# Optimization experiments

Hardware: AMD Instinct MI355X
Metric: run time of the kernel (lower is better)

Reference implementation:

```python
import jax, jax.numpy as jnp
import numpy as np

N_NODES = 100000
N_EDGES = 1600000
N_GRAPHS = 1000
D_IN = 64
D_HID = 64
D_OUT = 8


def _glorot(k, shape):
    lim = float(np.sqrt(6.0 / (shape[0] + shape[1])))
    return jax.random.uniform(k, shape, jnp.float32, -lim, lim)


def setup_inputs() -> dict:
    key = jax.random.key(0)
    ks = jax.random.split(key, 12)
    x = jax.random.normal(ks[0], (N_NODES, D_IN), jnp.float32)
    edge_index = jax.random.randint(ks[1], (2, N_EDGES), 0, N_NODES, jnp.int32)
    batch = jnp.sort(jax.random.randint(ks[2], (N_NODES,), 0, N_GRAPHS, jnp.int32))
    return {
        "x": x,
        "edge_index": edge_index,
        "batch": batch,
        "W1": _glorot(ks[3], (D_IN, D_HID)),
        "b1": jnp.zeros((D_HID,), jnp.float32),
        "W2": _glorot(ks[4], (D_HID, D_HID)),
        "b2": jnp.zeros((D_HID,), jnp.float32),
        "lw1": _glorot(ks[5], (D_HID, D_HID // 2)),
        "lb1": jnp.zeros((D_HID // 2,), jnp.float32),
        "lw2": _glorot(ks[6], (D_HID // 2, D_OUT)),
        "lb2": jnp.zeros((D_OUT,), jnp.float32),
    }


def reference(x, edge_index, batch, W1, b1, W2, b2, lw1, lb1, lw2, lb2):
    # --- GCN normalization (PyG defaults: add self-loops, sym norm) ---
    loop = jnp.arange(N_NODES, dtype=edge_index.dtype)
    src = jnp.concatenate([edge_index[0], loop])
    dst = jnp.concatenate([edge_index[1], loop])
    deg = jax.ops.segment_sum(jnp.ones_like(dst, jnp.float32), dst, num_segments=N_NODES)
    dinv = jnp.where(deg > 0, jax.lax.rsqrt(jnp.maximum(deg, 1.0)), 0.0)
    norm = dinv[src] * dinv[dst]  # [E+N]

    def gcn_conv(h, W, b):
        h = h @ W  # [N, d]
        msg = h[src] * norm[:, None]  # gather along edges
        return jax.ops.segment_sum(msg, dst, num_segments=N_NODES) + b

    h = jax.nn.relu(gcn_conv(x, W1, b1))
    h = gcn_conv(h, W2, b2)

    # --- global mean pool per graph ---
    counts = jax.ops.segment_sum(jnp.ones((N_NODES,), jnp.float32), batch, num_segments=N_GRAPHS)
    pooled = jax.ops.segment_sum(h, batch, num_segments=N_GRAPHS) / jnp.maximum(counts, 1.0)[:, None]

    # --- MLP head (dropout = identity in eval) ---
    z = jax.nn.relu(pooled @ lw1 + lb1)
    return z @ lw2 + lb2
```

## Files before the change

kernel.cpp:

```cpp
#include <hip/hip_runtime.h>

static constexpr int NN  = 100000;
static constexpr int NE  = 1600000;
static constexpr int NG  = 1000;
static constexpr int D   = 64;
static constexpr int DH  = 32;
static constexpr int DO  = 8;
static constexpr int BKT = 128;
static constexpr int NBK = (NN + BKT - 1) / BKT;
static constexpr int CHUNK = 4096;
static constexpr int NCH = (NE + CHUNK - 1) / CHUNK;

typedef __attribute__((ext_vector_type(8))) short bf16x8;
typedef __attribute__((ext_vector_type(4))) float f32x4;

__device__ __forceinline__ float b2f(unsigned short u) {
    return __uint_as_float(((unsigned int)u) << 16);
}
__device__ __forceinline__ unsigned short f2b(float f) {
    unsigned int u = __float_as_uint(f);
    u += 0x7FFFu + ((u >> 16) & 1u);
    return (unsigned short)(u >> 16);
}
__device__ __forceinline__ uint4 pack8(const unsigned short* h) {
    uint4 u;
    u.x = (unsigned)h[0] | ((unsigned)h[1] << 16);
    u.y = (unsigned)h[2] | ((unsigned)h[3] << 16);
    u.z = (unsigned)h[4] | ((unsigned)h[5] << 16);
    u.w = (unsigned)h[6] | ((unsigned)h[7] << 16);
    return u;
}

__global__ __launch_bounds__(512) void
k_hist(const int* __restrict__ dst, int* __restrict__ cntmat) {
    __shared__ int lcnt[NBK];
    int t = threadIdx.x;
    long base = (long)blockIdx.x * CHUNK;
    for (int b = t; b < NBK; b += 512) lcnt[b] = 0;
    __syncthreads();
#pragma unroll
    for (int j = 0; j < 8; ++j) {
        long i = base + j * 512 + t;
        if (i < NE) atomicAdd(&lcnt[dst[i] >> 7], 1);
    }
    __syncthreads();
    for (int b = t; b < NBK; b += 512)
        cntmat[blockIdx.x * NBK + b] = lcnt[b];
}

__global__ __launch_bounds__(512) void
k_colsum_rowscan(int* __restrict__ cntmat, int* __restrict__ bsum) {
    __shared__ int s[512];
    int b = blockIdx.x, t = threadIdx.x;
    int v = (t < NCH) ? cntmat[t * NBK + b] : 0;
    s[t] = v;
    __syncthreads();
    for (int o = 1; o < 512; o <<= 1) {
        int a = (t >= o) ? s[t - o] : 0;
        __syncthreads();
        s[t] += a;
        __syncthreads();
    }
    if (t < NCH) cntmat[t * NBK + b] = s[t] - v;
    if (t == 0) bsum[b] = s[511];
}

__global__ __launch_bounds__(1024) void
k_scan_prepw(const int* __restrict__ bsum, int* __restrict__ boffs,
             const float* __restrict__ W1, const float* __restrict__ W2,
             unsigned short* __restrict__ wtbuf) {
    int t = threadIdx.x;
    if (blockIdx.x == 0) {
        __shared__ int s[1024];
        int v = (t < NBK) ? bsum[t] : 0;
        s[t] = v;
        __syncthreads();
        for (int o = 1; o < 1024; o <<= 1) {
            int a = (t >= o) ? s[t - o] : 0;
            __syncthreads();
            s[t] += a;
            __syncthreads();
        }
        if (t < NBK) boffs[t] = s[t] - v;
        if (t == 0) boffs[NBK] = NE;
    } else if (t < 256) {
        const float* W = (blockIdx.x == 2) ? W2 : W1;
        unsigned short* WtHi = wtbuf + (size_t)(blockIdx.x - 1) * 8192;
        unsigned short* WtLo = WtHi + 4096;
        int n = t >> 2, k0 = (t & 3) * 16;
        unsigned short hi[16], lo[16];
#pragma unroll
        for (int i = 0; i < 16; ++i) {
            float v = W[(k0 + i) * 64 + n];
            hi[i] = f2b(v);
            lo[i] = f2b(v - b2f(hi[i]));
        }
        ((uint4*)WtHi)[n * 8 + (t & 3) * 2]     = pack8(hi);
        ((uint4*)WtHi)[n * 8 + (t & 3) * 2 + 1] = pack8(hi + 8);
        ((uint4*)WtLo)[n * 8 + (t & 3) * 2]     = pack8(lo);
        ((uint4*)WtLo)[n * 8 + (t & 3) * 2 + 1] = pack8(lo + 8);
    }
}

__global__ __launch_bounds__(512) void
k_bin(const int* __restrict__ src, const int* __restrict__ dst,
      const int* __restrict__ cntmat, const int* __restrict__ boffs,
      int* __restrict__ ebuf) {
    __shared__ int lcnt[NBK];
    __shared__ int lbase[NBK];
    int t = threadIdx.x;
    long base = (long)blockIdx.x * CHUNK;
    for (int b = t; b < NBK; b += 512) lcnt[b] = 0;
    __syncthreads();
    int pk[8], bk[8], of[8];
#pragma unroll
    for (int j = 0; j < 8; ++j) {
        long i = base + j * 512 + t;
        if (i < NE) {
            int d = dst[i];
            bk[j] = d >> 7;
            pk[j] = src[i] * BKT + (d & (BKT - 1));
            of[j] = atomicAdd(&lcnt[bk[j]], 1);
        } else bk[j] = -1;
    }
    __syncthreads();
    for (int b = t; b < NBK; b += 512)
        lbase[b] = cntmat[blockIdx.x * NBK + b] + boffs[b];
    __syncthreads();
#pragma unroll
    for (int j = 0; j < 8; ++j)
        if (bk[j] >= 0) ebuf[lbase[bk[j]] + of[j]] = pk[j];
}

__global__ __launch_bounds__(512) void
k_csrdeg(const int* __restrict__ boffs, const int* __restrict__ ebuf,
         int* __restrict__ rowptr, float* __restrict__ dinv, int* __restrict__ csr) {
    __shared__ int hist[BKT];
    __shared__ int sc[BKT];
    __shared__ int lcur[BKT];
    int b = blockIdx.x, t = threadIdx.x;
    if (t < BKT) hist[t] = 0;
    __syncthreads();
    int beg = boffs[b], end = boffs[b + 1];
    for (int e = beg + t; e < end; e += 512)
        atomicAdd(&hist[ebuf[e] & (BKT - 1)], 1);
    __syncthreads();
    if (t < BKT) sc[t] = hist[t];
    __syncthreads();
    for (int o = 1; o < BKT; o <<= 1) {
        int a = (t < BKT && t >= o) ? sc[t - o] : 0;
        __syncthreads();
        if (t < BKT) sc[t] += a;
        __syncthreads();
    }
    int v0 = b * BKT;
    if (t < BKT) {
        int v = v0 + t;
        if (v < NN) {
            int excl = beg + sc[t] - hist[t];
            rowptr[v] = excl;
            dinv[v]   = rsqrtf((float)(hist[t] + 1));
            lcur[t]   = excl;
        }
    }
    if (b == NBK - 1 && t == 0) rowptr[NN] = NE;
    __syncthreads();
    for (int e = beg + t; e < end; e += 512) {
        int p = ebuf[e];
        int slot = atomicAdd(&lcur[p & (BKT - 1)], 1);
        csr[slot] = p >> 7;
    }
}

template <bool SPLIT_A>
__global__ __launch_bounds__(256) void
k_mm_mfma(const void* __restrict__ Ain, const unsigned short* __restrict__ wt,
          const float* __restrict__ dinv, uint4* __restrict__ out) {
    __shared__ unsigned short smem[4 * 64 * 72];
    unsigned short* Ahi  = smem;
    unsigned short* Alo  = smem + 4608;
    unsigned short* WtHi = smem + 9216;
    unsigned short* WtLo = smem + 13824;
    int t = threadIdx.x;
    int r = t >> 2, cc = t & 3, c0 = cc * 16;
    long n0 = (long)blockIdx.x * 64;
    {
        const uint4* H = (const uint4*)wt;
        const uint4* L = (const uint4*)(wt + 4096);
        uint4* dh = (uint4*)&WtHi[r * 72 + c0];
        uint4* dl = (uint4*)&WtLo[r * 72 + c0];
        dh[0] = H[r * 8 + cc * 2]; dh[1] = H[r * 8 + cc * 2 + 1];
        dl[0] = L[r * 8 + cc * 2]; dl[1] = L[r * 8 + cc * 2 + 1];
    }
    {
        long n = n0 + r; if (n >= NN) n = NN - 1;
        if constexpr (SPLIT_A) {
            const float4* X = (const float4*)Ain;
            unsigned short hi[16], lo[16];
#pragma unroll
            for (int i = 0; i < 4; ++i) {
                float4 v = X[n * 16 + cc * 4 + i];
                float vv[4] = {v.x, v.y, v.z, v.w};
#pragma unroll
                for (int j = 0; j < 4; ++j) {
                    unsigned short h = f2b(vv[j]);
                    hi[i * 4 + j] = h;
                    lo[i * 4 + j] = f2b(vv[j] - b2f(h));
                }
            }
            uint4* dh = (uint4*)&Ahi[r * 72 + c0];
            uint4* dl = (uint4*)&Alo[r * 72 + c0];
            dh[0] = pack8(hi); dh[1] = pack8(hi + 8);
            dl[0] = pack8(lo); dl[1] = pack8(lo + 8);
        } else {
            const uint4* X = (const uint4*)Ain;
            uint4* dh = (uint4*)&Ahi[r * 72 + c0];
            dh[0] = X[n * 8 + cc * 2]; dh[1] = X[n * 8 + cc * 2 + 1];
        }
    }
    __syncthreads();
    int lane = t & 63, w = t >> 6;
    int q = lane >> 4, m = lane & 15;
    f32x4 acc[4] = {{0.f,0.f,0.f,0.f},{0.f,0.f,0.f,0.f},{0.f,0.f,0.f,0.f},{0.f,0.f,0.f,0.f}};
#pragma unroll
    for (int s = 0; s < 2; ++s) {
        int ko = s * 32 + q * 8;
        bf16x8 ah = *(const bf16x8*)&Ahi[(w * 16 + m) * 72 + ko];
        bf16x8 al{};
        if constexpr (SPLIT_A) al = *(const bf16x8*)&Alo[(w * 16 + m) * 72 + ko];
#pragma unroll
        for (int c = 0; c < 4; ++c) {
            bf16x8 bh = *(const bf16x8*)&WtHi[(c * 16 + m) * 72 + ko];
            bf16x8 bl = *(const bf16x8*)&WtLo[(c * 16 + m) * 72 + ko];
            acc[c] = __builtin_amdgcn_mfma_f32_16x16x32_bf16(ah, bh, acc[c], 0, 0, 0);
            acc[c] = __builtin_amdgcn_mfma_f32_16x16x32_bf16(ah, bl, acc[c], 0, 0, 0);
            if constexpr (SPLIT_A)
                acc[c] = __builtin_amdgcn_mfma_f32_16x16x32_bf16(al, bh, acc[c], 0, 0, 0);
        }
    }
    __syncthreads();
    float* Ct = (float*)smem;
#pragma unroll
    for (int c = 0; c < 4; ++c)
#pragma unroll
        for (int rr = 0; rr < 4; ++rr)
            Ct[(w * 16 + q * 4 + rr) * 68 + c * 16 + m] = acc[c][rr];
    __syncthreads();
    {
        long n = n0 + r;
        if (n < NN) {
            float dv = dinv[n];
            unsigned short ob[16];
#pragma unroll
            for (int i = 0; i < 4; ++i) {
                float4 v = *(const float4*)&Ct[r * 68 + c0 + i * 4];
                ob[i * 4 + 0] = f2b(v.x * dv); ob[i * 4 + 1] = f2b(v.y * dv);
                ob[i * 4 + 2] = f2b(v.z * dv); ob[i * 4 + 3] = f2b(v.w * dv);
            }
            out[n * 8 + cc * 2]     = pack8(ob);
            out[n * 8 + cc * 2 + 1] = pack8(ob + 8);
        }
    }
}

template <bool RELU>
__global__ __launch_bounds__(256) void
k_agg(const int* __restrict__ rowptr, const int* __restrict__ csr,
      const uint4* __restrict__ g4, const float* __restrict__ dinv,
      const float* __restrict__ bias, uint4* __restrict__ out4) {
    int t = threadIdx.x;
    int lane = t & 63;
    int fg = lane & 7;
    int slot = lane >> 3;
    int wid = blockIdx.x * 4 + (t >> 6);
    int v = wid * 8 + slot;
    int beg = rowptr[v];
    int len = rowptr[v + 1] - beg;
    int lmax = len;
    lmax = max(lmax, __shfl_xor(lmax, 8));
    lmax = max(lmax, __shfl_xor(lmax, 16));
    lmax = max(lmax, __shfl_xor(lmax, 32));
    float acc[8];
    {
        uint4 sv = g4[(long)v * 8 + fg];
        acc[0] = __uint_as_float(sv.x << 16); acc[1] = __uint_as_float(sv.x & 0xFFFF0000u);
        acc[2] = __uint_as_float(sv.y << 16); acc[3] = __uint_as_float(sv.y & 0xFFFF0000u);
        acc[4] = __uint_as_float(sv.z << 16); acc[5] = __uint_as_float(sv.z & 0xFFFF0000u);
        acc[6] = __uint_as_float(sv.w << 16); acc[7] = __uint_as_float(sv.w & 0xFFFF0000u);
    }
    for (int e = 0; e < lmax; e += 8) {
#pragma unroll
        for (int j = 0; j < 8; ++j) {
            int ee = e + j;
            float m = (ee < len) ? 1.f : 0.f;
            int idx = beg + ((ee < len) ? ee : 0);
            int srcn = csr[idx];
            uint4 a = g4[(long)srcn * 8 + fg];
            acc[0] += m * __uint_as_float(a.x << 16);
            acc[1] += m * __uint_as_float(a.x & 0xFFFF0000u);
            acc[2] += m * __uint_as_float(a.y << 16);
            acc[3] += m * __uint_as_float(a.y & 0xFFFF0000u);
            acc[4] += m * __uint_as_float(a.z << 16);
            acc[5] += m * __uint_as_float(a.z & 0xFFFF0000u);
            acc[6] += m * __uint_as_float(a.w << 16);
            acc[7] += m * __uint_as_float(a.w & 0xFFFF0000u);
        }
    }
    float dv = dinv[v];
    unsigned short ob[8];
#pragma unroll
    for (int k = 0; k < 8; ++k) {
        float x = acc[k] * dv + bias[fg * 8 + k];
        if (RELU) x = fmaxf(x, 0.f);
        ob[k] = f2b(x);
    }
    out4[(long)v * 8 + fg] = pack8(ob);
}

__global__ void k_poolhead(const unsigned short* __restrict__ h,
                           const int* __restrict__ batch,
                           const float* __restrict__ lw1, const float* __restrict__ lb1,
                           const float* __restrict__ lw2, const float* __restrict__ lb2,
                           float* __restrict__ out) {
    __shared__ float pl[D];
    __shared__ float z[DH];
    int g = blockIdx.x;
    int t = threadIdx.x;
    int lo = 0, hi = NN;
    while (lo < hi) { int m = (lo + hi) >> 1; if (batch[m] < g) lo = m + 1; else hi = m; }
    int lb = lo;
    hi = NN;
    while (lo < hi) { int m = (lo + hi) >> 1; if (batch[m] < g + 1) lo = m + 1; else hi = m; }
    int ub = lo;
    float s = 0.f;
    int n = lb;
    for (; n + 4 <= ub; n += 4) {
        float a0 = b2f(h[(long)(n + 0) * D + t]);
        float a1 = b2f(h[(long)(n + 1) * D + t]);
        float a2 = b2f(h[(long)(n + 2) * D + t]);
        float a3 = b2f(h[(long)(n + 3) * D + t]);
        s += a0 + a1 + a2 + a3;
    }
    for (; n < ub; ++n) s += b2f(h[(long)n * D + t]);
    pl[t] = s / fmaxf((float)(ub - lb), 1.0f);
    __syncthreads();
    if (t < DH) {
        float a = lb1[t];
#pragma unroll
        for (int k = 0; k < D; ++k) a += pl[k] * lw1[k * DH + t];
        z[t] = fmaxf(a, 0.f);
    }
    __syncthreads();
    if (t < DO) {
        float a = lb2[t];
#pragma unroll
        for (int j = 0; j < DH; ++j) a += z[j] * lw2[j * DO + t];
        out[g * DO + t] = a;
    }
}

extern "C" void kernel_launch(void* const* d_in, const int* in_sizes, int n_in,
                              void* d_out, int out_size, void* d_ws, size_t ws_size,
                              hipStream_t stream) {
    const float* x    = (const float*)d_in[0];
    const int*   ei   = (const int*)  d_in[1];
    const int*   batch= (const int*)  d_in[2];
    const float* W1   = (const float*)d_in[3];
    const float* b1   = (const float*)d_in[4];
    const float* W2   = (const float*)d_in[5];
    const float* b2   = (const float*)d_in[6];
    const float* lw1  = (const float*)d_in[7];
    const float* lb1  = (const float*)d_in[8];
    const float* lw2  = (const float*)d_in[9];
    const float* lb2  = (const float*)d_in[10];
    float* out = (float*)d_out;

    const int* srcv = ei;
    const int* dstv = ei + NE;

    char* ws = (char*)d_ws;
    size_t off = 0;
    auto alloc = [&](size_t bytes) {
        void* p = ws + off;
        off = (off + bytes + 255) & ~(size_t)255;
        return p;
    };
    int*   cntmat = (int*)  alloc((size_t)NCH * NBK * 4);
    int*   bsum   = (int*)  alloc((size_t)NBK * 4);
    int*   boffs  = (int*)  alloc((size_t)(NBK + 1) * 4);
    int*   rowptr = (int*)  alloc((size_t)(NN + 1) * 4);
    int*   csr    = (int*)  alloc((size_t)NE * 4);
    float* dinv   = (float*)alloc((size_t)NN * 4);
    unsigned short* wtbuf = (unsigned short*)alloc((size_t)4 * 4096 * 2);
    unsigned short* bufA = (unsigned short*)alloc((size_t)NN * D * 2);
    unsigned short* bufB = (unsigned short*)alloc((size_t)NN * D * 2);
    int*   ebuf   = (int*)bufA;

    k_hist          <<<NCH, 512, 0, stream>>>(dstv, cntmat);
    k_colsum_rowscan<<<NBK, 512, 0, stream>>>(cntmat, bsum);
    k_scan_prepw    <<<3, 1024, 0, stream>>>(bsum, boffs, W1, W2, wtbuf);
    k_bin           <<<NCH, 512, 0, stream>>>(srcv, dstv, cntmat, boffs, ebuf);
    k_csrdeg        <<<NBK, 512, 0, stream>>>(boffs, ebuf, rowptr, dinv, csr);

    const int MMB = (NN + 63) / 64;

    k_mm_mfma<true><<<MMB, 256, 0, stream>>>(x, wtbuf, dinv, (uint4*)bufA);
    k_agg<true><<<NN / 32, 256, 0, stream>>>(
        rowptr, csr, (const uint4*)bufA, dinv, b1, (uint4*)bufB);

    k_mm_mfma<false><<<MMB, 256, 0, stream>>>(bufB, wtbuf + 8192, dinv, (uint4*)bufA);
    k_agg<false><<<NN / 32, 256, 0, stream>>>(
        rowptr, csr, (const uint4*)bufA, dinv, b2, (uint4*)bufB);

    k_poolhead<<<NG, 64, 0, stream>>>(bufB, batch, lw1, lb1, lw2, lb2, out);
}
```

Before: 225.4 us.

## Merge CSR build into cooperative kernel and fuse layer-1 aggregation with layer-2 matmul

The five CSR-construction kernels (histogram, column scan, bucket offsets, binning, per-bucket sort and degree) become one cooperative kernel that uses grid-wide syncs, which removes several launch gaps. The first aggregation is fused with the second layer's MFMA matmul, so the ReLU'd hidden features stay in LDS and are never written to and re-read from global memory. This cuts launch overhead and one full feature round trip. In exchange it relies on a cooperative launch of 391 blocks of 512 threads all being resident at once, grid.sync costs, and a 512-thread fused kernel whose occupancy may be lower than before.

```diff
diff --git a/kernel.cpp b/kernel.cpp
--- a/kernel.cpp
+++ b/kernel.cpp
@@ -1,4 +1,7 @@
 #include <hip/hip_runtime.h>
+#include <hip/hip_cooperative_groups.h>
+
+namespace cg = cooperative_groups;
 
 static constexpr int NN  = 100000;
 static constexpr int NE  = 1600000;
@@ -32,60 +35,64 @@
 }
 
 __global__ __launch_bounds__(512) void
-k_hist(const int* __restrict__ dst, int* __restrict__ cntmat) {
-    __shared__ int lcnt[NBK];
-    int t = threadIdx.x;
-    long base = (long)blockIdx.x * CHUNK;
-    for (int b = t; b < NBK; b += 512) lcnt[b] = 0;
-    __syncthreads();
-#pragma unroll
-    for (int j = 0; j < 8; ++j) {
-        long i = base + j * 512 + t;
-        if (i < NE) atomicAdd(&lcnt[dst[i] >> 7], 1);
-    }
-    __syncthreads();
-    for (int b = t; b < NBK; b += 512)
-        cntmat[blockIdx.x * NBK + b] = lcnt[b];
-}
-
-__global__ __launch_bounds__(512) void
-k_colsum_rowscan(int* __restrict__ cntmat, int* __restrict__ bsum) {
-    __shared__ int s[512];
-    int b = blockIdx.x, t = threadIdx.x;
-    int v = (t < NCH) ? cntmat[t * NBK + b] : 0;
-    s[t] = v;
-    __syncthreads();
-    for (int o = 1; o < 512; o <<= 1) {
-        int a = (t >= o) ? s[t - o] : 0;
-        __syncthreads();
-        s[t] += a;
-        __syncthreads();
-    }
-    if (t < NCH) cntmat[t * NBK + b] = s[t] - v;
-    if (t == 0) bsum[b] = s[511];
-}
-
-__global__ __launch_bounds__(1024) void
-k_scan_prepw(const int* __restrict__ bsum, int* __restrict__ boffs,
-             const float* __restrict__ W1, const float* __restrict__ W2,
-             unsigned short* __restrict__ wtbuf) {
-    int t = threadIdx.x;
-    if (blockIdx.x == 0) {
-        __shared__ int s[1024];
-        int v = (t < NBK) ? bsum[t] : 0;
-        s[t] = v;
+k_prep(const int* __restrict__ src, const int* __restrict__ dst,
+       const float* __restrict__ W1, const float* __restrict__ W2,
+       int* __restrict__ cntmat, int* __restrict__ bsum, int* __restrict__ boffs,
+       unsigned short* __restrict__ wtbuf, int* __restrict__ ebuf,
+       int* __restrict__ rowptr, float* __restrict__ dinv, int* __restrict__ csr) {
+    cg::grid_group grid = cg::this_grid();
+    __shared__ int sh[1568];
+    int t = threadIdx.x, blk = blockIdx.x;
+
+    {
+        for (int b = t; b < NBK; b += 512) sh[b] = 0;
+        __syncthreads();
+        long base = (long)blk * CHUNK;
+#pragma unroll
+        for (int j = 0; j < 8; ++j) {
+            long i = base + j * 512 + t;
+            if (i < NE) atomicAdd(&sh[dst[i] >> 7], 1);
+        }
+        __syncthreads();
+        for (int b = t; b < NBK; b += 512) cntmat[blk * NBK + b] = sh[b];
+    }
+    grid.sync();
+
+    for (int bb = 0; bb < 2; ++bb) {
+        int b = blk + bb * 391;
+        int v = (t < NCH) ? cntmat[t * NBK + b] : 0;
+        __syncthreads();
+        sh[t] = v;
+        __syncthreads();
+        for (int o = 1; o < 512; o <<= 1) {
+            int a = (t >= o) ? sh[t - o] : 0;
+            __syncthreads();
+            sh[t] += a;
+            __syncthreads();
+        }
+        if (t < NCH) cntmat[t * NBK + b] = sh[t] - v;
+        if (t == 0) bsum[b] = sh[511];
+    }
+    grid.sync();
+
+    if (blk == 0) {
+        int v0 = (t < NBK) ? bsum[t] : 0;
+        int v1 = (t + 512 < NBK) ? bsum[t + 512] : 0;
+        sh[t] = v0; sh[t + 512] = v1;
         __syncthreads();
         for (int o = 1; o < 1024; o <<= 1) {
-            int a = (t >= o) ? s[t - o] : 0;
+            int a0 = (t >= o) ? sh[t - o] : 0;
+            int a1 = sh[t + 512 - o];
             __syncthreads();
-            s[t] += a;
+            sh[t] += a0; sh[t + 512] += a1;
             __syncthreads();
         }
-        if (t < NBK) boffs[t] = s[t] - v;
+        if (t < NBK) boffs[t] = sh[t] - v0;
+        if (t + 512 < NBK) boffs[t + 512] = sh[t + 512] - v1;
         if (t == 0) boffs[NBK] = NE;
-    } else if (t < 256) {
-        const float* W = (blockIdx.x == 2) ? W2 : W1;
-        unsigned short* WtHi = wtbuf + (size_t)(blockIdx.x - 1) * 8192;
+    } else if (blk <= 2 && t < 256) {
+        const float* W = (blk == 2) ? W2 : W1;
+        unsigned short* WtHi = wtbuf + (size_t)(blk - 1) * 8192;
         unsigned short* WtLo = WtHi + 4096;
         int n = t >> 2, k0 = (t & 3) * 16;
         unsigned short hi[16], lo[16];
@@ -100,81 +107,77 @@
         ((uint4*)WtLo)[n * 8 + (t & 3) * 2]     = pack8(lo);
         ((uint4*)WtLo)[n * 8 + (t & 3) * 2 + 1] = pack8(lo + 8);
     }
-}
-
-__global__ __launch_bounds__(512) void
-k_bin(const int* __restrict__ src, const int* __restrict__ dst,
-      const int* __restrict__ cntmat, const int* __restrict__ boffs,
-      int* __restrict__ ebuf) {
-    __shared__ int lcnt[NBK];
-    __shared__ int lbase[NBK];
-    int t = threadIdx.x;
-    long base = (long)blockIdx.x * CHUNK;
-    for (int b = t; b < NBK; b += 512) lcnt[b] = 0;
-    __syncthreads();
-    int pk[8], bk[8], of[8];
-#pragma unroll
-    for (int j = 0; j < 8; ++j) {
-        long i = base + j * 512 + t;
-        if (i < NE) {
-            int d = dst[i];
-            bk[j] = d >> 7;
-            pk[j] = src[i] * BKT + (d & (BKT - 1));
-            of[j] = atomicAdd(&lcnt[bk[j]], 1);
-        } else bk[j] = -1;
-    }
-    __syncthreads();
-    for (int b = t; b < NBK; b += 512)
-        lbase[b] = cntmat[blockIdx.x * NBK + b] + boffs[b];
-    __syncthreads();
-#pragma unroll
-    for (int j = 0; j < 8; ++j)
-        if (bk[j] >= 0) ebuf[lbase[bk[j]] + of[j]] = pk[j];
-}
-
-__global__ __launch_bounds__(512) void
-k_csrdeg(const int* __restrict__ boffs, const int* __restrict__ ebuf,
-         int* __restrict__ rowptr, float* __restrict__ dinv, int* __restrict__ csr) {
-    __shared__ int hist[BKT];
-    __shared__ int sc[BKT];
-    __shared__ int lcur[BKT];
-    int b = blockIdx.x, t = threadIdx.x;
-    if (t < BKT) hist[t] = 0;
-    __syncthreads();
-    int beg = boffs[b], end = boffs[b + 1];
-    for (int e = beg + t; e < end; e += 512)
-        atomicAdd(&hist[ebuf[e] & (BKT - 1)], 1);
-    __syncthreads();
-    if (t < BKT) sc[t] = hist[t];
-    __syncthreads();
-    for (int o = 1; o < BKT; o <<= 1) {
-        int a = (t < BKT && t >= o) ? sc[t - o] : 0;
-        __syncthreads();
-        if (t < BKT) sc[t] += a;
-        __syncthreads();
-    }
-    int v0 = b * BKT;
-    if (t < BKT) {
-        int v = v0 + t;
-        if (v < NN) {
-            int excl = beg + sc[t] - hist[t];
-            rowptr[v] = excl;
-            dinv[v]   = rsqrtf((float)(hist[t] + 1));
-            lcur[t]   = excl;
-        }
-    }
-    if (b == NBK - 1 && t == 0) rowptr[NN] = NE;
-    __syncthreads();
-    for (int e = beg + t; e < end; e += 512) {
-        int p = ebuf[e];
-        int slot = atomicAdd(&lcur[p & (BKT - 1)], 1);
-        csr[slot] = p >> 7;
-    }
-}
-
-template <bool SPLIT_A>
+    grid.sync();
+
+    {
+        int* lcnt  = sh;
+        int* lbase = sh + 784;
+        for (int b = t; b < NBK; b += 512) lcnt[b] = 0;
+        __syncthreads();
+        long base = (long)blk * CHUNK;
+        int pk[8], bk[8], of[8];
+#pragma unroll
+        for (int j = 0; j < 8; ++j) {
+            long i = base + j * 512 + t;
+            if (i < NE) {
+                int d = dst[i];
+                bk[j] = d >> 7;
+                pk[j] = src[i] * BKT + (d & (BKT - 1));
+                of[j] = atomicAdd(&lcnt[bk[j]], 1);
+            } else bk[j] = -1;
+        }
+        __syncthreads();
+        for (int b = t; b < NBK; b += 512)
+            lbase[b] = cntmat[blk * NBK + b] + boffs[b];
+        __syncthreads();
+#pragma unroll
+        for (int j = 0; j < 8; ++j)
+            if (bk[j] >= 0) ebuf[lbase[bk[j]] + of[j]] = pk[j];
+    }
+    grid.sync();
+
+    for (int bb = 0; bb < 2; ++bb) {
+        int b = blk + bb * 391;
+        int* hist = sh;
+        int* sc   = sh + 128;
+        int* lcur = sh + 256;
+        __syncthreads();
+        if (t < BKT) hist[t] = 0;
+        __syncthreads();
+        int beg = boffs[b], end = boffs[b + 1];
+        for (int e = beg + t; e < end; e += 512)
+            atomicAdd(&hist[ebuf[e] & (BKT - 1)], 1);
+        __syncthreads();
+        if (t < BKT) sc[t] = hist[t];
+        __syncthreads();
+        for (int o = 1; o < BKT; o <<= 1) {
+            int a = (t < BKT && t >= o) ? sc[t - o] : 0;
+            __syncthreads();
+            if (t < BKT) sc[t] += a;
+            __syncthreads();
+        }
+        int v0 = b * BKT;
+        if (t < BKT) {
+            int v = v0 + t;
+            if (v < NN) {
+                int excl = beg + sc[t] - hist[t];
+                rowptr[v] = excl;
+                dinv[v]   = rsqrtf((float)(hist[t] + 1));
+                lcur[t]   = excl;
+            }
+        }
+        if (b == NBK - 1 && t == 0) rowptr[NN] = NE;
+        __syncthreads();
+        for (int e = beg + t; e < end; e += 512) {
+            int p = ebuf[e];
+            int slot = atomicAdd(&lcur[p & (BKT - 1)], 1);
+            csr[slot] = p >> 7;
+        }
+    }
+}
+
 __global__ __launch_bounds__(256) void
-k_mm_mfma(const void* __restrict__ Ain, const unsigned short* __restrict__ wt,
+k_mm_mfma(const float* __restrict__ Ain, const unsigned short* __restrict__ wt,
           const float* __restrict__ dinv, uint4* __restrict__ out) {
     __shared__ unsigned short smem[4 * 64 * 72];
     unsigned short* Ahi  = smem;
@@ -194,29 +197,23 @@
     }
     {
         long n = n0 + r; if (n >= NN) n = NN - 1;
-        if constexpr (SPLIT_A) {
-            const float4* X = (const float4*)Ain;
-            unsigned short hi[16], lo[16];
-#pragma unroll
-            for (int i = 0; i < 4; ++i) {
-                float4 v = X[n * 16 + cc * 4 + i];
-                float vv[4] = {v.x, v.y, v.z, v.w};
-#pragma unroll
-                for (int j = 0; j < 4; ++j) {
-                    unsigned short h = f2b(vv[j]);
-                    hi[i * 4 + j] = h;
-                    lo[i * 4 + j] = f2b(vv[j] - b2f(h));
-                }
+        const float4* X = (const float4*)Ain;
+        unsigned short hi[16], lo[16];
+#pragma unroll
+        for (int i = 0; i < 4; ++i) {
+            float4 v = X[n * 16 + cc * 4 + i];
+            float vv[4] = {v.x, v.y, v.z, v.w};
+#pragma unroll
+            for (int j = 0; j < 4; ++j) {
+                unsigned short h = f2b(vv[j]);
+                hi[i * 4 + j] = h;
+                lo[i * 4 + j] = f2b(vv[j] - b2f(h));
             }
-            uint4* dh = (uint4*)&Ahi[r * 72 + c0];
-            uint4* dl = (uint4*)&Alo[r * 72 + c0];
-            dh[0] = pack8(hi); dh[1] = pack8(hi + 8);
-            dl[0] = pack8(lo); dl[1] = pack8(lo + 8);
-        } else {
-            const uint4* X = (const uint4*)Ain;
-            uint4* dh = (uint4*)&Ahi[r * 72 + c0];
-            dh[0] = X[n * 8 + cc * 2]; dh[1] = X[n * 8 + cc * 2 + 1];
-        }
+        }
+        uint4* dh = (uint4*)&Ahi[r * 72 + c0];
+        uint4* dl = (uint4*)&Alo[r * 72 + c0];
+        dh[0] = pack8(hi); dh[1] = pack8(hi + 8);
+        dl[0] = pack8(lo); dl[1] = pack8(lo + 8);
     }
     __syncthreads();
     int lane = t & 63, w = t >> 6;
@@ -226,16 +223,14 @@
     for (int s = 0; s < 2; ++s) {
         int ko = s * 32 + q * 8;
         bf16x8 ah = *(const bf16x8*)&Ahi[(w * 16 + m) * 72 + ko];
-        bf16x8 al{};
-        if constexpr (SPLIT_A) al = *(const bf16x8*)&Alo[(w * 16 + m) * 72 + ko];
+        bf16x8 al = *(const bf16x8*)&Alo[(w * 16 + m) * 72 + ko];
 #pragma unroll
         for (int c = 0; c < 4; ++c) {
             bf16x8 bh = *(const bf16x8*)&WtHi[(c * 16 + m) * 72 + ko];
             bf16x8 bl = *(const bf16x8*)&WtLo[(c * 16 + m) * 72 + ko];
             acc[c] = __builtin_amdgcn_mfma_f32_16x16x32_bf16(ah, bh, acc[c], 0, 0, 0);
             acc[c] = __builtin_amdgcn_mfma_f32_16x16x32_bf16(ah, bl, acc[c], 0, 0, 0);
-            if constexpr (SPLIT_A)
-                acc[c] = __builtin_amdgcn_mfma_f32_16x16x32_bf16(al, bh, acc[c], 0, 0, 0);
+            acc[c] = __builtin_amdgcn_mfma_f32_16x16x32_bf16(al, bh, acc[c], 0, 0, 0);
         }
     }
     __syncthreads();
@@ -263,26 +258,42 @@
     }
 }
 
-template <bool RELU>
-__global__ __launch_bounds__(256) void
-k_agg(const int* __restrict__ rowptr, const int* __restrict__ csr,
-      const uint4* __restrict__ g4, const float* __restrict__ dinv,
-      const float* __restrict__ bias, uint4* __restrict__ out4) {
+__global__ __launch_bounds__(512) void
+k_aggmm(const int* __restrict__ rowptr, const int* __restrict__ csr,
+        const uint4* __restrict__ g4, const float* __restrict__ dinv,
+        const float* __restrict__ bias, const unsigned short* __restrict__ wt,
+        uint4* __restrict__ out) {
+    __shared__ unsigned short smem[3 * 4608];
+    unsigned short* Ahi  = smem;
+    unsigned short* WtHi = smem + 4608;
+    unsigned short* WtLo = smem + 9216;
     int t = threadIdx.x;
-    int lane = t & 63;
-    int fg = lane & 7;
-    int slot = lane >> 3;
-    int wid = blockIdx.x * 4 + (t >> 6);
-    int v = wid * 8 + slot;
-    int beg = rowptr[v];
-    int len = rowptr[v + 1] - beg;
+    long n0 = (long)blockIdx.x * 64;
+    if (t < 256) {
+        int r = t >> 2, cc = t & 3, c0 = cc * 16;
+        const uint4* H = (const uint4*)wt;
+        const uint4* L = (const uint4*)(wt + 4096);
+        uint4* dh = (uint4*)&WtHi[r * 72 + c0];
+        uint4* dl = (uint4*)&WtLo[r * 72 + c0];
+        dh[0] = H[r * 8 + cc * 2]; dh[1] = H[r * 8 + cc * 2 + 1];
+        dl[0] = L[r * 8 + cc * 2]; dl[1] = L[r * 8 + cc * 2 + 1];
+    }
+    int lane = t & 63, w = t >> 6;
+    int fg = lane & 7, slot = lane >> 3;
+    int ln = w * 8 + slot;
+    long v = n0 + ln;
+    int vc = (v < NN) ? (int)v : NN - 1;
+    int beg = rowptr[vc];
+    int len = rowptr[vc + 1] - beg;
+    if (v >= NN) len = 0;
     int lmax = len;
     lmax = max(lmax, __shfl_xor(lmax, 8));
     lmax = max(lmax, __shfl_xor(lmax, 16));
     lmax = max(lmax, __shfl_xor(lmax, 32));
     float acc[8];
     {
-        uint4 sv = g4[(long)v * 8 + fg];
+        uint4 sv = g4[(long)vc * 8 + fg];
+        if (v >= NN) { sv.x = sv.y = sv.z = sv.w = 0u; }
         acc[0] = __uint_as_float(sv.x << 16); acc[1] = __uint_as_float(sv.x & 0xFFFF0000u);
         acc[2] = __uint_as_float(sv.y << 16); acc[3] = __uint_as_float(sv.y & 0xFFFF0000u);
         acc[4] = __uint_as_float(sv.z << 16); acc[5] = __uint_as_float(sv.z & 0xFFFF0000u);
@@ -306,14 +317,102 @@
             acc[7] += m * __uint_as_float(a.w & 0xFFFF0000u);
         }
     }
+    {
+        float dv = dinv[vc];
+        unsigned short ob[8];
+#pragma unroll
+        for (int k = 0; k < 8; ++k) {
+            float x = fmaxf(acc[k] * dv + bias[fg * 8 + k], 0.f);
+            ob[k] = f2b(x);
+        }
+        *(uint4*)&Ahi[ln * 72 + fg * 8] = pack8(ob);
+    }
+    __syncthreads();
+    int q = lane >> 4, m = lane & 15;
+    int rs = (w & 3) * 16;
+    int cb0 = (w >> 2) * 2;
+    f32x4 c2[2] = {{0.f,0.f,0.f,0.f},{0.f,0.f,0.f,0.f}};
+#pragma unroll
+    for (int s = 0; s < 2; ++s) {
+        int ko = s * 32 + q * 8;
+        bf16x8 ah = *(const bf16x8*)&Ahi[(rs + m) * 72 + ko];
+#pragma unroll
+        for (int c = 0; c < 2; ++c) {
+            bf16x8 bh = *(const bf16x8*)&WtHi[((cb0 + c) * 16 + m) * 72 + ko];
+            bf16x8 bl = *(const bf16x8*)&WtLo[((cb0 + c) * 16 + m) * 72 + ko];
+            c2[c] = __builtin_amdgcn_mfma_f32_16x16x32_bf16(ah, bh, c2[c], 0, 0, 0);
+            c2[c] = __builtin_amdgcn_mfma_f32_16x16x32_bf16(ah, bl, c2[c], 0, 0, 0);
+        }
+    }
+    __syncthreads();
+    float* Ct = (float*)smem;
+#pragma unroll
+    for (int c = 0; c < 2; ++c)
+#pragma unroll
+        for (int rr = 0; rr < 4; ++rr)
+            Ct[(rs + q * 4 + rr) * 68 + (cb0 + c) * 16 + m] = c2[c][rr];
+    __syncthreads();
+    {
+        int r = t >> 3, c8 = (t & 7) * 8;
+        long n = n0 + r;
+        if (n < NN) {
+            float dv = dinv[n];
+            float4 a = *(const float4*)&Ct[r * 68 + c8];
+            float4 b = *(const float4*)&Ct[r * 68 + c8 + 4];
+            unsigned short ob[8] = {f2b(a.x * dv), f2b(a.y * dv), f2b(a.z * dv), f2b(a.w * dv),
+                                    f2b(b.x * dv), f2b(b.y * dv), f2b(b.z * dv), f2b(b.w * dv)};
+            out[n * 8 + (t & 7)] = pack8(ob);
+        }
+    }
+}
+
+__global__ __launch_bounds__(256) void
+k_agg2(const int* __restrict__ rowptr, const int* __restrict__ csr,
+       const uint4* __restrict__ g4, const float* __restrict__ dinv,
+       const float* __restrict__ bias, uint4* __restrict__ out4) {
+    int t = threadIdx.x;
+    int lane = t & 63;
+    int fg = lane & 7;
+    int slot = lane >> 3;
+    int wid = blockIdx.x * 4 + (t >> 6);
+    int v = wid * 8 + slot;
+    int beg = rowptr[v];
+    int len = rowptr[v + 1] - beg;
+    int lmax = len;
+    lmax = max(lmax, __shfl_xor(lmax, 8));
+    lmax = max(lmax, __shfl_xor(lmax, 16));
+    lmax = max(lmax, __shfl_xor(lmax, 32));
+    float acc[8];
+    {
+        uint4 sv = g4[(long)v * 8 + fg];
+        acc[0] = __uint_as_float(sv.x << 16); acc[1] = __uint_as_float(sv.x & 0xFFFF0000u);
+        acc[2] = __uint_as_float(sv.y << 16); acc[3] = __uint_as_float(sv.y & 0xFFFF0000u);
+        acc[4] = __uint_as_float(sv.z << 16); acc[5] = __uint_as_float(sv.z & 0xFFFF0000u);
+        acc[6] = __uint_as_float(sv.w << 16); acc[7] = __uint_as_float(sv.w & 0xFFFF0000u);
+    }
+    for (int e = 0; e < lmax; e += 8) {
+#pragma unroll
+        for (int j = 0; j < 8; ++j) {
+            int ee = e + j;
+            float m = (ee < len) ? 1.f : 0.f;
+            int idx = beg + ((ee < len) ? ee : 0);
+            int srcn = csr[idx];
+            uint4 a = g4[(long)srcn * 8 + fg];
+            acc[0] += m * __uint_as_float(a.x << 16);
+            acc[1] += m * __uint_as_float(a.x & 0xFFFF0000u);
+            acc[2] += m * __uint_as_float(a.y << 16);
+            acc[3] += m * __uint_as_float(a.y & 0xFFFF0000u);
+            acc[4] += m * __uint_as_float(a.z << 16);
+            acc[5] += m * __uint_as_float(a.z & 0xFFFF0000u);
+            acc[6] += m * __uint_as_float(a.w << 16);
+            acc[7] += m * __uint_as_float(a.w & 0xFFFF0000u);
+        }
+    }
     float dv = dinv[v];
     unsigned short ob[8];
 #pragma unroll
-    for (int k = 0; k < 8; ++k) {
-        float x = acc[k] * dv + bias[fg * 8 + k];
-        if (RELU) x = fmaxf(x, 0.f);
-        ob[k] = f2b(x);
-    }
+    for (int k = 0; k < 8; ++k)
+        ob[k] = f2b(acc[k] * dv + bias[fg * 8 + k]);
     out4[(long)v * 8 + fg] = pack8(ob);
 }
 
@@ -396,21 +495,20 @@
     unsigned short* bufB = (unsigned short*)alloc((size_t)NN * D * 2);
     int*   ebuf   = (int*)bufA;
 
-    k_hist          <<<NCH, 512, 0, stream>>>(dstv, cntmat);
-    k_colsum_rowscan<<<NBK, 512, 0, stream>>>(cntmat, bsum);
-    k_scan_prepw    <<<3, 1024, 0, stream>>>(bsum, boffs, W1, W2, wtbuf);
-    k_bin           <<<NCH, 512, 0, stream>>>(srcv, dstv, cntmat, boffs, ebuf);
-    k_csrdeg        <<<NBK, 512, 0, stream>>>(boffs, ebuf, rowptr, dinv, csr);
+    {
+        void* args[] = {(void*)&srcv, (void*)&dstv, (void*)&W1, (void*)&W2,
+                        (void*)&cntmat, (void*)&bsum, (void*)&boffs, (void*)&wtbuf,
+                        (void*)&ebuf, (void*)&rowptr, (void*)&dinv, (void*)&csr};
+        hipLaunchCooperativeKernel((const void*)k_prep, dim3(NCH), dim3(512),
+                                   args, 0, stream);
+    }
 
     const int MMB = (NN + 63) / 64;
 
-    k_mm_mfma<true><<<MMB, 256, 0, stream>>>(x, wtbuf, dinv, (uint4*)bufA);
-    k_agg<true><<<NN / 32, 256, 0, stream>>>(
-        rowptr, csr, (const uint4*)bufA, dinv, b1, (uint4*)bufB);
-
-    k_mm_mfma<false><<<MMB, 256, 0, stream>>>(bufB, wtbuf + 8192, dinv, (uint4*)bufA);
-    k_agg<false><<<NN / 32, 256, 0, stream>>>(
-        rowptr, csr, (const uint4*)bufA, dinv, b2, (uint4*)bufB);
-
-    k_poolhead<<<NG, 64, 0, stream>>>(bufB, batch, lw1, lb1, lw2, lb2, out);
-}
+    k_mm_mfma<<<MMB, 256, 0, stream>>>(x, wtbuf, dinv, (uint4*)bufA);
+    k_aggmm<<<MMB, 512, 0, stream>>>(rowptr, csr, (const uint4*)bufA, dinv, b1,
+                                     wtbuf + 8192, (uint4*)bufB);
+    k_agg2<<<NN / 32, 256, 0, stream>>>(rowptr, csr, (const uint4*)bufB, dinv, b2,
+                                        (uint4*)bufA);
+    k_poolhead<<<NG, 64, 0, stream>>>(bufA, batch, lw1, lb1, lw2, lb2, out);
+}
```

Result: slower. 437.2 us (+94.0%).
